# Optimization experiments

Hardware: AMD Instinct MI355X
Metric: run time of the kernel (lower is better)

Reference implementation:

```python
import jax, jax.numpy as jnp
import numpy as np

B = 256
H, W = 8, 16          # input_resolution for channels=256
C = 768               # dim = channels*3
WS = 4                # window_size
SHIFT = 2             # shift_size
NH = 12               # num_heads
HD = C // NH          # head_dim = 64
HID = 1024            # mlp hidden = channels*4
N = WS * WS           # tokens per window = 16
NW = (H // WS) * (W // WS)  # windows per image = 8
LN_EPS = 1e-5


def _rel_pos_index():
    coords = np.stack(np.meshgrid(np.arange(WS), np.arange(WS), indexing='ij'))  # [2,ws,ws]
    cf = coords.reshape(2, -1)                      # [2, N]
    rel = (cf[:, :, None] - cf[:, None, :]).transpose(1, 2, 0)  # [N, N, 2]
    rel[:, :, 0] += WS - 1
    rel[:, :, 1] += WS - 1
    rel[:, :, 0] *= 2 * WS - 1
    return jnp.asarray(rel.sum(-1))                 # [N, N] int


def _attn_mask():
    img = np.zeros((H, W))
    slices = (slice(0, -WS), slice(-WS, -SHIFT), slice(-SHIFT, None))
    cnt = 0
    for hs in slices:
        for ws_ in slices:
            img[hs, ws_] = cnt
            cnt += 1
    mw = img.reshape(H // WS, WS, W // WS, WS).transpose(0, 2, 1, 3).reshape(-1, N)  # [nW, N]
    am = mw[:, None, :] - mw[:, :, None]            # [nW, N, N]
    return jnp.asarray(np.where(am != 0, -100.0, 0.0).astype(np.float32))


REL_IDX = _rel_pos_index()
ATTN_MASK = _attn_mask()


def _ln(x, g, b):
    m = x.mean(-1, keepdims=True)
    v = ((x - m) ** 2).mean(-1, keepdims=True)
    return (x - m) / jnp.sqrt(v + LN_EPS) * g + b


def setup_inputs() -> dict:
    key = jax.random.key(0)
    ks = jax.random.split(key, 8)
    s = 0.02
    return {
        'x': jax.random.normal(ks[0], (B, H * W, C), jnp.float32),
        'ln1_g': jnp.ones((C,), jnp.float32),
        'ln1_b': jnp.zeros((C,), jnp.float32),
        'qkv_w': jax.random.normal(ks[1], (C, 3 * C), jnp.float32) * s,
        'qkv_b': jnp.zeros((3 * C,), jnp.float32),
        'proj_w': jax.random.normal(ks[2], (C, C), jnp.float32) * s,
        'proj_b': jnp.zeros((C,), jnp.float32),
        'rel_table': jax.random.normal(ks[3], ((2 * WS - 1) * (2 * WS - 1), NH), jnp.float32) * s,
        'ln2_g': jnp.ones((C,), jnp.float32),
        'ln2_b': jnp.zeros((C,), jnp.float32),
        'fc1_w': jax.random.normal(ks[4], (C, HID), jnp.float32) * s,
        'fc1_b': jax.random.normal(ks[5], (HID,), jnp.float32) * 1e-6,
        'fc2_w': jax.random.normal(ks[6], (HID, C), jnp.float32) * s,
        'fc2_b': jax.random.normal(ks[7], (C,), jnp.float32) * 1e-6,
    }


def reference(x, ln1_g, ln1_b, qkv_w, qkv_b, proj_w, proj_b, rel_table,
              ln2_g, ln2_b, fc1_w, fc1_b, fc2_w, fc2_b):
    # --- norm1 + cyclic shift + window partition ---
    h = _ln(x, ln1_g, ln1_b).reshape(B, H, W, C)
    h = jnp.roll(h, (-SHIFT, -SHIFT), axis=(1, 2))
    hw = h.reshape(B, H // WS, WS, W // WS, WS, C).transpose(0, 1, 3, 2, 4, 5)
    hw = hw.reshape(B * NW, N, C)                   # (num_windows*B, N, C)
    # --- window attention with relative position bias + shift mask ---
    qkv = (hw @ qkv_w + qkv_b).reshape(B * NW, N, 3, NH, HD).transpose(2, 0, 3, 1, 4)
    q, k, v = qkv[0] * (HD ** -0.5), qkv[1], qkv[2]  # [Bn, NH, N, HD]
    attn = jnp.einsum('bhnd,bhmd->bhnm', q, k)      # [Bn, NH, N, N]
    bias = rel_table[REL_IDX].transpose(2, 0, 1)    # [NH, N, N]
    attn = attn + bias[None]
    attn = attn.reshape(B, NW, NH, N, N) + ATTN_MASK[None, :, None]
    attn = jax.nn.softmax(attn.reshape(B * NW, NH, N, N), axis=-1)
    o = jnp.einsum('bhnm,bhmd->bhnd', attn, v).transpose(0, 2, 1, 3).reshape(B * NW, N, C)
    o = o @ proj_w + proj_b
    # --- window reverse + reverse shift + residual ---
    o = o.reshape(B, H // WS, W // WS, WS, WS, C).transpose(0, 1, 3, 2, 4, 5).reshape(B, H, W, C)
    o = jnp.roll(o, (SHIFT, SHIFT), axis=(1, 2)).reshape(B, H * W, C)
    x = x + o
    # --- MLP block (dropout is identity at inference) ---
    y = _ln(x, ln2_g, ln2_b)
    y = jax.nn.gelu(y @ fc1_w + fc1_b, approximate=False)
    return x + (y @ fc2_w + fc2_b)
```

## Files before the change

### kernel.cpp

```cpp
#include <hip/hip_runtime.h>
#include <stdint.h>
#include <stddef.h>

typedef __attribute__((ext_vector_type(8))) short bf16x8;
typedef __attribute__((ext_vector_type(4))) float f32x4;
typedef __attribute__((ext_vector_type(4))) unsigned int uint4v;

static __device__ __forceinline__ unsigned short f2bf(float f) {
  unsigned int u = __builtin_bit_cast(unsigned int, f);
  unsigned int r = (u + 0x7FFFu + ((u >> 16) & 1u)) >> 16;
  return (unsigned short)r;
}

static __device__ __forceinline__ void gld16(const void* g, void* l) {
  __builtin_amdgcn_global_load_lds(
      (const __attribute__((address_space(1))) void*)g,
      (__attribute__((address_space(3))) void*)l, 16, 0, 0);
}

__global__ void transpose_cast(const float* __restrict__ src,
                               unsigned short* __restrict__ dst, int R, int C) {
  __shared__ float tile[32][33];
  int c0 = blockIdx.x * 32, r0 = blockIdx.y * 32;
  int tx = threadIdx.x, ty = threadIdx.y;
  #pragma unroll
  for (int i = 0; i < 32; i += 8)
    tile[ty + i][tx] = src[(size_t)(r0 + ty + i) * C + c0 + tx];
  __syncthreads();
  #pragma unroll
  for (int i = 0; i < 32; i += 8)
    dst[(size_t)(c0 + ty + i) * R + r0 + tx] = f2bf(tile[tx][ty + i]);
}

static __device__ __forceinline__ float blksum256(float v, float* sb) {
  #pragma unroll
  for (int o = 32; o > 0; o >>= 1) v += __shfl_down(v, o, 64);
  int lane = threadIdx.x & 63, w = threadIdx.x >> 6;
  __syncthreads();
  if (lane == 0) sb[w] = v;
  __syncthreads();
  return sb[0] + sb[1] + sb[2] + sb[3];
}

template <int MODE>
__global__ __launch_bounds__(256) void ln_kernel(const float* __restrict__ x,
                                                 const float* __restrict__ gg,
                                                 const float* __restrict__ bb,
                                                 unsigned short* __restrict__ out) {
  __shared__ float sb[4];
  const int d = blockIdx.x;
  size_t srow;
  if (MODE == 0) {
    int b = d >> 7, wid = (d >> 4) & 7, tok = d & 15;
    int oh = (((wid >> 2) << 2) + (tok >> 2) + 2) & 7;
    int ow = (((wid & 3) << 2) + (tok & 3) + 2) & 15;
    srow = (size_t)(b << 7) + oh * 16 + ow;
  } else {
    srow = d;
  }
  const float* xr = x + srow * 768;
  const int t = threadIdx.x;
  float v0 = xr[t], v1 = xr[t + 256], v2 = xr[t + 512];
  float mean = blksum256(v0 + v1 + v2, sb) * (1.0f / 768.0f);
  float d0 = v0 - mean, d1 = v1 - mean, d2 = v2 - mean;
  float var = blksum256(d0 * d0 + d1 * d1 + d2 * d2, sb) * (1.0f / 768.0f);
  float rstd = rsqrtf(var + 1e-5f);
  size_t o = (size_t)d * 768;
  out[o + t]       = f2bf(d0 * rstd * gg[t] + bb[t]);
  out[o + t + 256] = f2bf(d1 * rstd * gg[t + 256] + bb[t + 256]);
  out[o + t + 512] = f2bf(d2 * rstd * gg[t + 512] + bb[t + 512]);
}

template <int EPI>
__global__ __launch_bounds__(512, 2) void gemm256(
    const unsigned short* __restrict__ A, const unsigned short* __restrict__ BT,
    const float* __restrict__ bias, float* __restrict__ outF,
    unsigned short* __restrict__ outB, const float* __restrict__ resid,
    int M, int N, int K, int NT) {
  __shared__ __align__(16) unsigned short sA[2][256 * 64];
  __shared__ __align__(16) unsigned short sB[2][256 * 64];

  const int tid = threadIdx.x;
  const int lane = tid & 63, wv = tid >> 6;
  const int wr = wv >> 2, wc = wv & 3;
  const int fr = lane & 15, q4 = (lane >> 4) << 2;

  const int nwg = gridDim.x;
  const int orig = blockIdx.x;
  const int swz = (orig & 7) * (nwg >> 3) + (orig >> 3);
  const int mt = swz / NT, nt = swz - mt * NT;
  const int m0 = mt << 8, n0 = nt << 8;

  const size_t K2 = (size_t)K * 2;

  const int srow = tid >> 3;
  const int sg = tid & 7;
  const int sgs = ((sg ^ (srow & 7)) << 4);
  const char* pA = (const char*)A + (size_t)(m0 + srow) * K2 + sgs;
  const char* pB = (const char*)BT + (size_t)(n0 + srow) * K2 + sgs;
  char* lwA[2] = {(char*)&sA[0][0] + (wv << 10), (char*)&sA[1][0] + (wv << 10)};
  char* lwB[2] = {(char*)&sB[0][0] + (wv << 10), (char*)&sB[1][0] + (wv << 10)};

  const int g0 = (((lane >> 4) ^ (fr & 7)) << 4);
  const int g1 = (((4 + (lane >> 4)) ^ (fr & 7)) << 4);
  const int arow = (wr << 7) + fr;
  const int brow = (wc << 6) + fr;

  f32x4 acc[8][4];
  #pragma unroll
  for (int i = 0; i < 8; ++i)
    #pragma unroll
    for (int j = 0; j < 4; ++j) acc[i][j] = (f32x4){0.f, 0.f, 0.f, 0.f};

  bf16x8 af[4][2], bb[2][2];
  const int KT = K >> 6;

#define STAGE(la, lb, t)                                                   \
  {                                                                        \
    const size_t koff = (size_t)(t) << 7;                                  \
    _Pragma("unroll") for (int j = 0; j < 4; ++j) {                        \
      gld16(pA + (size_t)(j * 64) * K2 + koff, (la) + j * 8192);           \
      gld16(pB + (size_t)(j * 64) * K2 + koff, (lb) + j * 8192);           \
    }                                                                      \
  }

#define LDA(cbuf, mh)                                                      \
  {                                                                        \
    const char* bas = (const char*)&sA[cbuf][0];                           \
    _Pragma("unroll") for (int fm = 0; fm < 4; ++fm) {                     \
      const int r = arow + (mh) * 64 + fm * 16;                            \
      af[fm][0] = *(const bf16x8*)(bas + r * 128 + g0);                    \
      af[fm][1] = *(const bf16x8*)(bas + r * 128 + g1);                    \
    }                                                                      \
  }

#define LDB(cbuf, nh)                                                      \
  {                                                                        \
    const char* bas = (const char*)&sB[cbuf][0];                           \
    _Pragma("unroll") for (int fn = 0; fn < 2; ++fn) {                     \
      const int r = brow + (nh) * 32 + fn * 16;                            \
      bb[fn][0] = *(const bf16x8*)(bas + r * 128 + g0);                    \
      bb[fn][1] = *(const bf16x8*)(bas + r * 128 + g1);                    \
    }                                                                      \
  }

#define MMA(mh, nh)                                                        \
  {                                                                        \
    __builtin_amdgcn_s_barrier();                                          \
    __builtin_amdgcn_s_setprio(1);                                         \
    _Pragma("unroll") for (int fm = 0; fm < 4; ++fm) {                     \
      _Pragma("unroll") for (int fn = 0; fn < 2; ++fn) {                   \
        acc[(mh)*4 + fm][(nh)*2 + fn] =                                    \
            __builtin_amdgcn_mfma_f32_16x16x32_bf16(                       \
                af[fm][0], bb[fn][0], acc[(mh)*4 + fm][(nh)*2 + fn], 0, 0, 0); \
        acc[(mh)*4 + fm][(nh)*2 + fn] =                                    \
            __builtin_amdgcn_mfma_f32_16x16x32_bf16(                       \
                af[fm][1], bb[fn][1], acc[(mh)*4 + fm][(nh)*2 + fn], 0, 0, 0); \
      }                                                                    \
    }                                                                      \
    __builtin_amdgcn_s_setprio(0);                                         \
    __builtin_amdgcn_s_barrier();                                          \
  }

  STAGE(lwA[0], lwB[0], 0);
  STAGE(lwA[1], lwB[1], 1);
  asm volatile("s_waitcnt vmcnt(8)" ::: "memory");
  __builtin_amdgcn_s_barrier();

  for (int t = 0; t < KT; ++t) {
    const int cur = t & 1;
    LDA(cur, 0) LDB(cur, 0) MMA(0, 0)
    LDB(cur, 1) MMA(0, 1)
    LDA(cur, 1) MMA(1, 1)
    LDB(cur, 0) MMA(1, 0)
    if (t + 2 < KT) {
      STAGE(lwA[cur], lwB[cur], t + 2);
      asm volatile("s_waitcnt vmcnt(8)" ::: "memory");
    } else {
      asm volatile("s_waitcnt vmcnt(0)" ::: "memory");
    }
    __builtin_amdgcn_s_barrier();
  }
#undef STAGE
#undef LDA
#undef LDB
#undef MMA

  #pragma unroll
  for (int ai = 0; ai < 8; ++ai) {
    #pragma unroll
    for (int bj = 0; bj < 4; ++bj) {
      const int col = n0 + (wc << 6) + bj * 16 + fr;
      const float bc = bias[col];
      #pragma unroll
      for (int i = 0; i < 4; ++i) {
        const int row = m0 + (wr << 7) + ai * 16 + q4 + i;
        float v = acc[ai][bj][i] + bc;
        if (EPI == 0) {
          outB[(size_t)row * N + col] = f2bf(v);
        } else if (EPI == 1) {
          int b = row >> 7, wid = (row >> 4) & 7, tok = row & 15;
          int oh = (((wid >> 2) << 2) + (tok >> 2) + 2) & 7;
          int ow = (((wid & 3) << 2) + (tok & 3) + 2) & 15;
          size_t di = ((size_t)(b << 7) + oh * 16 + ow) * 768 + col;
          outF[di] = v + resid[di];
        } else if (EPI == 2) {
          float g = 0.5f * v * (1.0f + erff(v * 0.70710678118f));
          outB[(size_t)row * N + col] = f2bf(g);
        } else {
          size_t di = (size_t)row * N + col;
          outF[di] = v + resid[di];
        }
      }
    }
  }
}

__global__ __launch_bounds__(64) void attn_win(const unsigned short* __restrict__ qkv,
                                               const float* __restrict__ rel_table,
                                               unsigned short* __restrict__ o) {
  __shared__ __align__(16) unsigned short q_s[16 * 64];
  __shared__ __align__(16) unsigned short k_s[16 * 64];
  __shared__ __align__(16) unsigned short vt_s[64 * 32];
  __shared__ __align__(16) unsigned short p_s[16 * 32];
  const int bid = blockIdx.x;
  const int win = bid / 12;
  const int head = bid - win * 12;
  const int wid = win & 7;
  const int lane = threadIdx.x;
  const unsigned short* gq =
      qkv + (size_t)win * 16 * 2304 + head * 64 + (size_t)(lane >> 2) * 2304 + ((lane & 3) << 4);
  const int t = lane >> 2, d0 = (lane & 3) << 4;
  *(uint4v*)&q_s[t * 64 + d0]     = *(const uint4v*)(gq);
  *(uint4v*)&q_s[t * 64 + d0 + 8] = *(const uint4v*)(gq + 8);
  *(uint4v*)&k_s[t * 64 + d0]     = *(const uint4v*)(gq + 768);
  *(uint4v*)&k_s[t * 64 + d0 + 8] = *(const uint4v*)(gq + 776);
  unsigned short vv[16];
  *(uint4v*)&vv[0] = *(const uint4v*)(gq + 1536);
  *(uint4v*)&vv[8] = *(const uint4v*)(gq + 1544);
  #pragma unroll
  for (int e = 0; e < 16; ++e) vt_s[(d0 + e) * 32 + t] = vv[e];
  #pragma unroll
  for (int e = 0; e < 16; ++e) vt_s[lane * 32 + 16 + e] = 0;
  if (lane < 16) {
    #pragma unroll
    for (int e = 0; e < 16; ++e) p_s[lane * 32 + 16 + e] = 0;
  }
  __syncthreads();

  const int fr = lane & 15, kg = (lane >> 4) << 3;
  bf16x8 qa0 = *(const bf16x8*)&q_s[fr * 64 + kg];
  bf16x8 qa1 = *(const bf16x8*)&q_s[fr * 64 + 32 + kg];
  bf16x8 ka0 = *(const bf16x8*)&k_s[fr * 64 + kg];
  bf16x8 ka1 = *(const bf16x8*)&k_s[fr * 64 + 32 + kg];
  f32x4 s = (f32x4){0.f, 0.f, 0.f, 0.f};
  s = __builtin_amdgcn_mfma_f32_16x16x32_bf16(qa0, ka0, s, 0, 0, 0);
  s = __builtin_amdgcn_mfma_f32_16x16x32_bf16(qa1, ka1, s, 0, 0, 0);

  const int wh = wid >> 2, wwc = wid & 3;
  const int rj = fr >> 2, cj = fr & 3;
  const int rowm = wh * 4 + rj, colm = wwc * 4 + cj;
  const int rgm = (rowm < 4 ? 0 : (rowm < 6 ? 1 : 2)) * 3 +
                  (colm < 12 ? 0 : (colm < 14 ? 1 : 2));
  float p[4];
  #pragma unroll
  for (int i = 0; i < 4; ++i) {
    int n = ((lane >> 4) << 2) + i;
    int ri = n >> 2, ci = n & 3;
    int rown = wh * 4 + ri, coln = wwc * 4 + ci;
    int rgn = (rown < 4 ? 0 : (rown < 6 ? 1 : 2)) * 3 +
              (coln < 12 ? 0 : (coln < 14 ? 1 : 2));
    float bias = rel_table[(size_t)((ri - rj + 3) * 7 + (ci - cj + 3)) * 12 + head];
    p[i] = s[i] * 0.125f + bias + (rgn != rgm ? -100.0f : 0.0f);
  }
  float mx[4] = {p[0], p[1], p[2], p[3]};
  #pragma unroll
  for (int off = 8; off > 0; off >>= 1)
    #pragma unroll
    for (int i = 0; i < 4; ++i) mx[i] = fmaxf(mx[i], __shfl_xor(mx[i], off, 64));
  float sm[4];
  #pragma unroll
  for (int i = 0; i < 4; ++i) { p[i] = __expf(p[i] - mx[i]); sm[i] = p[i]; }
  #pragma unroll
  for (int off = 8; off > 0; off >>= 1)
    #pragma unroll
    for (int i = 0; i < 4; ++i) sm[i] += __shfl_xor(sm[i], off, 64);
  #pragma unroll
  for (int i = 0; i < 4; ++i)
    p_s[(((lane >> 4) << 2) + i) * 32 + fr] = f2bf(p[i] / sm[i]);
  __syncthreads();

  bf16x8 pa = *(const bf16x8*)&p_s[fr * 32 + kg];
  const f32x4 oz = (f32x4){0.f, 0.f, 0.f, 0.f};
  #pragma unroll
  for (int c = 0; c < 4; ++c) {
    bf16x8 vb = *(const bf16x8*)&vt_s[(c * 16 + fr) * 32 + kg];
    f32x4 oa = __builtin_amdgcn_mfma_f32_16x16x32_bf16(pa, vb, oz, 0, 0, 0);
    #pragma unroll
    for (int i = 0; i < 4; ++i) {
      int n = ((lane >> 4) << 2) + i;
      o[((size_t)win * 16 + n) * 768 + head * 64 + c * 16 + fr] = f2bf(oa[i]);
    }
  }
}

extern "C" void kernel_launch(void* const* d_in, const int* in_sizes, int n_in,
                              void* d_out, int out_size, void* d_ws, size_t ws_size,
                              hipStream_t stream) {
  const float* x      = (const float*)d_in[0];
  const float* ln1_g  = (const float*)d_in[1];
  const float* ln1_b  = (const float*)d_in[2];
  const float* qkv_w  = (const float*)d_in[3];
  const float* qkv_b  = (const float*)d_in[4];
  const float* proj_w = (const float*)d_in[5];
  const float* proj_b = (const float*)d_in[6];
  const float* rel_t  = (const float*)d_in[7];
  const float* ln2_g  = (const float*)d_in[8];
  const float* ln2_b  = (const float*)d_in[9];
  const float* fc1_w  = (const float*)d_in[10];
  const float* fc1_b  = (const float*)d_in[11];
  const float* fc2_w  = (const float*)d_in[12];
  const float* fc2_b  = (const float*)d_in[13];
  float* out = (float*)d_out;

  char* ws = (char*)d_ws;
  unsigned short* wsA = (unsigned short*)(ws);
  unsigned short* qkvb = (unsigned short*)(ws + 50331648);
  float* xr = (float*)(ws + 50331648);
  unsigned short* h1 = (unsigned short*)(ws + 201326592);
  unsigned short* qkv_wT = (unsigned short*)(ws + 268435456);
  unsigned short* proj_wT = (unsigned short*)(ws + 271974400);
  unsigned short* fc1_wT = (unsigned short*)(ws + 273154048);
  unsigned short* fc2_wT = (unsigned short*)(ws + 274726912);

  dim3 tb(32, 8);
  transpose_cast<<<dim3(2304 / 32, 768 / 32), tb, 0, stream>>>(qkv_w, qkv_wT, 768, 2304);
  transpose_cast<<<dim3(768 / 32, 768 / 32), tb, 0, stream>>>(proj_w, proj_wT, 768, 768);
  transpose_cast<<<dim3(1024 / 32, 768 / 32), tb, 0, stream>>>(fc1_w, fc1_wT, 768, 1024);
  transpose_cast<<<dim3(768 / 32, 1024 / 32), tb, 0, stream>>>(fc2_w, fc2_wT, 1024, 768);

  ln_kernel<0><<<32768, 256, 0, stream>>>(x, ln1_g, ln1_b, wsA);
  gemm256<0><<<dim3(128 * 9), 512, 0, stream>>>(wsA, qkv_wT, qkv_b, nullptr, qkvb,
                                                nullptr, 32768, 2304, 768, 9);
  attn_win<<<24576, 64, 0, stream>>>(qkvb, rel_t, wsA);
  gemm256<1><<<dim3(128 * 3), 512, 0, stream>>>(wsA, proj_wT, proj_b, xr, nullptr,
                                                x, 32768, 768, 768, 3);
  ln_kernel<1><<<32768, 256, 0, stream>>>(xr, ln2_g, ln2_b, wsA);
  gemm256<2><<<dim3(128 * 4), 512, 0, stream>>>(wsA, fc1_wT, fc1_b, nullptr, h1,
                                                nullptr, 32768, 1024, 768, 4);
  gemm256<3><<<dim3(128 * 3), 512, 0, stream>>>(h1, fc2_wT, fc2_b, out, nullptr,
                                                xr, 32768, 768, 1024, 3);
}
```

Before: 616.8 us.

## Interleave global-to-LDS staging with MFMA quadrants in unrolled double-buffered GEMM loop

Reworks the bf16 GEMM main loop to unroll two K-tiles per iteration and spread the global_load_lds stage loads one chunk at a time between the four MFMA quadrants. B fragments are kept per half so that one LDB can be reused. Sched barriers and explicit lgkmcnt/vmcnt waits pin the ordering. The goal is to hide global load latency behind compute and to avoid issuing a burst of loads after compute. The cost is a more fragile schedule, and correctness now relies on KT being even and on the finer-grained waits.

```diff
diff --git a/kernel.cpp b/kernel.cpp
--- a/kernel.cpp
+++ b/kernel.cpp
@@ -98,8 +98,8 @@
   const int sgs = ((sg ^ (srow & 7)) << 4);
   const char* pA = (const char*)A + (size_t)(m0 + srow) * K2 + sgs;
   const char* pB = (const char*)BT + (size_t)(n0 + srow) * K2 + sgs;
-  char* lwA[2] = {(char*)&sA[0][0] + (wv << 10), (char*)&sA[1][0] + (wv << 10)};
-  char* lwB[2] = {(char*)&sB[0][0] + (wv << 10), (char*)&sB[1][0] + (wv << 10)};
+  char* sdA = (char*)&sA[0][0] + (wv << 10);
+  char* sdB = (char*)&sB[0][0] + (wv << 10);
 
   const int g0 = (((lane >> 4) ^ (fr & 7)) << 4);
   const int g1 = (((4 + (lane >> 4)) ^ (fr & 7)) << 4);
@@ -112,79 +112,99 @@
     #pragma unroll
     for (int j = 0; j < 4; ++j) acc[i][j] = (f32x4){0.f, 0.f, 0.f, 0.f};
 
-  bf16x8 af[4][2], bb[2][2];
+  bf16x8 af[4][2];
+  bf16x8 bbv[2][2][2];
   const int KT = K >> 6;
-
-#define STAGE(la, lb, t)                                                   \
-  {                                                                        \
-    const size_t koff = (size_t)(t) << 7;                                  \
-    _Pragma("unroll") for (int j = 0; j < 4; ++j) {                        \
-      gld16(pA + (size_t)(j * 64) * K2 + koff, (la) + j * 8192);           \
-      gld16(pB + (size_t)(j * 64) * K2 + koff, (lb) + j * 8192);           \
-    }                                                                      \
-  }
-
-#define LDA(cbuf, mh)                                                      \
-  {                                                                        \
-    const char* bas = (const char*)&sA[cbuf][0];                           \
-    _Pragma("unroll") for (int fm = 0; fm < 4; ++fm) {                     \
-      const int r = arow + (mh) * 64 + fm * 16;                            \
-      af[fm][0] = *(const bf16x8*)(bas + r * 128 + g0);                    \
-      af[fm][1] = *(const bf16x8*)(bas + r * 128 + g1);                    \
-    }                                                                      \
-  }
-
-#define LDB(cbuf, nh)                                                      \
-  {                                                                        \
-    const char* bas = (const char*)&sB[cbuf][0];                           \
-    _Pragma("unroll") for (int fn = 0; fn < 2; ++fn) {                     \
-      const int r = brow + (nh) * 32 + fn * 16;                            \
-      bb[fn][0] = *(const bf16x8*)(bas + r * 128 + g0);                    \
-      bb[fn][1] = *(const bf16x8*)(bas + r * 128 + g1);                    \
-    }                                                                      \
-  }
-
-#define MMA(mh, nh)                                                        \
-  {                                                                        \
-    __builtin_amdgcn_s_barrier();                                          \
-    __builtin_amdgcn_s_setprio(1);                                         \
-    _Pragma("unroll") for (int fm = 0; fm < 4; ++fm) {                     \
-      _Pragma("unroll") for (int fn = 0; fn < 2; ++fn) {                   \
-        acc[(mh)*4 + fm][(nh)*2 + fn] =                                    \
-            __builtin_amdgcn_mfma_f32_16x16x32_bf16(                       \
-                af[fm][0], bb[fn][0], acc[(mh)*4 + fm][(nh)*2 + fn], 0, 0, 0); \
-        acc[(mh)*4 + fm][(nh)*2 + fn] =                                    \
-            __builtin_amdgcn_mfma_f32_16x16x32_bf16(                       \
-                af[fm][1], bb[fn][1], acc[(mh)*4 + fm][(nh)*2 + fn], 0, 0, 0); \
-      }                                                                    \
-    }                                                                      \
-    __builtin_amdgcn_s_setprio(0);                                         \
-    __builtin_amdgcn_s_barrier();                                          \
-  }
-
-  STAGE(lwA[0], lwB[0], 0);
-  STAGE(lwA[1], lwB[1], 1);
-  asm volatile("s_waitcnt vmcnt(8)" ::: "memory");
-  __builtin_amdgcn_s_barrier();
-
-  for (int t = 0; t < KT; ++t) {
-    const int cur = t & 1;
-    LDA(cur, 0) LDB(cur, 0) MMA(0, 0)
-    LDB(cur, 1) MMA(0, 1)
-    LDA(cur, 1) MMA(1, 1)
-    LDB(cur, 0) MMA(1, 0)
-    if (t + 2 < KT) {
-      STAGE(lwA[cur], lwB[cur], t + 2);
-      asm volatile("s_waitcnt vmcnt(8)" ::: "memory");
-    } else {
-      asm volatile("s_waitcnt vmcnt(0)" ::: "memory");
-    }
-    __builtin_amdgcn_s_barrier();
-  }
-#undef STAGE
+  const int NI = KT >> 1;
+
+#define BARR __builtin_amdgcn_s_barrier()
+#define SCB __builtin_amdgcn_sched_barrier(0)
+#define LGKM0 asm volatile("s_waitcnt lgkmcnt(0)" ::: "memory")
+#define VM2 asm volatile("s_waitcnt vmcnt(2)" ::: "memory")
+#define VM0 asm volatile("s_waitcnt vmcnt(0)" ::: "memory")
+
+#define LDA(CB, mh)                                                          \
+  {                                                                          \
+    const char* ba = ((const char*)&sA[0][0]) + (CB)*32768;                  \
+    _Pragma("unroll") for (int fm = 0; fm < 4; ++fm) {                       \
+      const int r = arow + (mh)*64 + fm * 16;                                \
+      af[fm][0] = *(const bf16x8*)(ba + r * 128 + g0);                       \
+      af[fm][1] = *(const bf16x8*)(ba + r * 128 + g1);                       \
+    }                                                                        \
+  }
+#define LDB(CB, nh)                                                          \
+  {                                                                          \
+    const char* ba = ((const char*)&sB[0][0]) + (CB)*32768;                  \
+    _Pragma("unroll") for (int fn = 0; fn < 2; ++fn) {                       \
+      const int r = brow + (nh)*32 + fn * 16;                                \
+      bbv[nh][fn][0] = *(const bf16x8*)(ba + r * 128 + g0);                  \
+      bbv[nh][fn][1] = *(const bf16x8*)(ba + r * 128 + g1);                  \
+    }                                                                        \
+  }
+#define STG(CB, tt, j)                                                       \
+  {                                                                          \
+    const size_t ko = (size_t)(tt) << 7;                                     \
+    gld16(pA + (size_t)((j)*64) * K2 + ko, sdA + (CB)*32768 + (j)*8192);     \
+    gld16(pB + (size_t)((j)*64) * K2 + ko, sdB + (CB)*32768 + (j)*8192);     \
+  }
+#define MMAQ(mh, nh)                                                         \
+  _Pragma("unroll") for (int fm = 0; fm < 4; ++fm)                           \
+      _Pragma("unroll") for (int fn = 0; fn < 2; ++fn) {                     \
+    f32x4* ac = &acc[(mh)*4 + fm][(nh)*2 + fn];                              \
+    *ac = __builtin_amdgcn_mfma_f32_16x16x32_bf16(af[fm][0], bbv[nh][fn][0], \
+                                                  *ac, 0, 0, 0);             \
+    *ac = __builtin_amdgcn_mfma_f32_16x16x32_bf16(af[fm][1], bbv[nh][fn][1], \
+                                                  *ac, 0, 0, 0);             \
+  }
+#define OPEN  SCB; BARR; LGKM0; SCB; __builtin_amdgcn_s_setprio(1)
+#define OPEN_NOLD  SCB; BARR; __builtin_amdgcn_s_setprio(1)
+#define CLOSE __builtin_amdgcn_s_setprio(0)
+
+  #pragma unroll
+  for (int j = 0; j < 4; ++j) STG(0, 0, j);
+  STG(1, 1, 0);
+  VM2;
+  BARR;
+
+  for (int i = 0; i < NI; ++i) {
+    const int s1 = 2 * i + 1, s2 = 2 * i + 2, s3 = 2 * i + 3;
+    const bool gl = (i + 1 < NI);
+    LDB(0, 0) LDA(0, 0) STG(1, s1, 1)
+    OPEN; MMAQ(0, 0); CLOSE; BARR;
+    LDB(0, 1) STG(1, s1, 2)
+    OPEN; MMAQ(0, 1); CLOSE; BARR;
+    LDA(0, 1) STG(1, s1, 3)
+    OPEN; MMAQ(1, 1); CLOSE; BARR;
+    if (gl) STG(0, s2, 0)
+    OPEN_NOLD; MMAQ(1, 0); CLOSE;
+    if (gl) { VM2; } else { VM0; }
+    BARR;
+    LDB(1, 0) LDA(1, 0)
+    if (gl) STG(0, s2, 1)
+    OPEN; MMAQ(0, 0); CLOSE; BARR;
+    LDB(1, 1)
+    if (gl) STG(0, s2, 2)
+    OPEN; MMAQ(0, 1); CLOSE; BARR;
+    LDA(1, 1)
+    if (gl) STG(0, s2, 3)
+    OPEN; MMAQ(1, 1); CLOSE; BARR;
+    if (gl) STG(1, s3, 0)
+    OPEN_NOLD; MMAQ(1, 0); CLOSE;
+    if (gl) { VM2; } else { VM0; }
+    BARR;
+  }
+#undef BARR
+#undef SCB
+#undef LGKM0
+#undef VM2
+#undef VM0
 #undef LDA
 #undef LDB
-#undef MMA
+#undef STG
+#undef MMAQ
+#undef OPEN
+#undef OPEN_NOLD
+#undef CLOSE
 
   #pragma unroll
   for (int ai = 0; ai < 8; ++ai) {
```

Result: faster. 580.4 us (-5.9%).
